# Kernel optimization log

Hardware: AMD Instinct MI355X
Metric: run time of the kernel (lower is better)

## Reference

```python
import jax, jax.numpy as jnp
import numpy as np

B, N = 16, 128
DN0, DE0, DH = 64, 16, 128  # input node dim, input edge dim, hidden dim


def _gnn2(A, x, e, w_msg, b_msg, w_node, b_node):
    """One GNN2 layer on dense batched graphs.
    A: [B,N,N] adjacency mask, x: [B,N,Dn], e: [B,N,N,De].
    Message/new-edge: relu(Linear([x_i, x_j, e_ij])) masked by A.
    New node: relu(Linear([x, sum_j msg_ij])).
    The concat-Linear is decomposed into three matmuls to avoid
    materializing the [B,N,N,2Dn+De] concat tensor.
    """
    Dn = x.shape[-1]
    Wi, Wj, We = w_msg[:Dn], w_msg[Dn:2 * Dn], w_msg[2 * Dn:]
    xi = x @ Wi                                   # [B,N,Do]
    xj = x @ Wj                                   # [B,N,Do]
    msg = jax.nn.relu(xi[:, :, None, :] + xj[:, None, :, :] + e @ We + b_msg)
    msg = msg * A[..., None]                      # mask non-edges -> new edge_attr [B,N,N,Do]
    agg = msg.sum(axis=2)                         # scatter-sum over neighbors j -> [B,N,Do]
    Wx, Wa = w_node[:Dn], w_node[Dn:]
    x_new = jax.nn.relu(x @ Wx + agg @ Wa + b_node)
    return x_new, msg


def setup_inputs() -> dict:
    key = jax.random.key(0)
    ks = iter(jax.random.split(key, 32))
    s = 0.05
    inp = {
        "edge_index": jax.random.randint(next(ks), (B, N, N), 0, 2, dtype=jnp.int32),
        "x": jax.random.normal(next(ks), (B, N, DN0), dtype=jnp.float32),
        "edge_attr": jax.random.normal(next(ks), (B, N, N, DE0), dtype=jnp.float32),
    }
    def w(shape):
        return s * jax.random.normal(next(ks), shape, dtype=jnp.float32)
    # layer 0: node_in=64, edge_in=16 -> 128
    inp["w_msg_0"], inp["b_msg_0"] = w((2 * DN0 + DE0, DH)), w((DH,))
    inp["w_node_0"], inp["b_node_0"] = w((DN0 + DH, DH)), w((DH,))
    # layers 1,2: 128 -> 128
    for l in (1, 2):
        inp[f"w_msg_{l}"], inp[f"b_msg_{l}"] = w((2 * DH + DH, DH)), w((DH,))
        inp[f"w_node_{l}"], inp[f"b_node_{l}"] = w((DH + DH, DH)), w((DH,))
    # head mlp: 128 -> 128 -> 128 -> 1
    inp["w_h1"], inp["b_h1"] = w((DH, DH)), w((DH,))
    inp["w_h2"], inp["b_h2"] = w((DH, DH)), w((DH,))
    inp["w_h3"], inp["b_h3"] = w((DH, 1)), w((1,))
    return inp


def reference(edge_index, x, edge_attr,
              w_msg_0, b_msg_0, w_node_0, b_node_0,
              w_msg_1, b_msg_1, w_node_1, b_node_1,
              w_msg_2, b_msg_2, w_node_2, b_node_2,
              w_h1, b_h1, w_h2, b_h2, w_h3, b_h3):
    A = edge_index.astype(jnp.float32)
    x = x.astype(jnp.float32)
    # layer 0
    x, e = _gnn2(A, x, edge_attr, w_msg_0, b_msg_0, w_node_0, b_node_0)
    # middle layer with 0.5 residual blend
    x_, e_ = _gnn2(A, x, e, w_msg_1, b_msg_1, w_node_1, b_node_1)
    x = 0.5 * (x + x_)
    e = 0.5 * (e + e_)
    # last layer
    x, e = _gnn2(A, x, e, w_msg_2, b_msg_2, w_node_2, b_node_2)
    # edge_mean readout + MLP head
    h = e.mean(axis=(1, 2))                       # [B, DH]
    h = jax.nn.relu(h @ w_h1 + b_h1)
    h = jax.nn.relu(h @ w_h2 + b_h2)
    out = h @ w_h3 + b_h3                         # [B, 1]
    return out.squeeze(-1)                        # [B]
```

## Files before the change

### kernel.cpp

```cpp
#include <hip/hip_runtime.h>

constexpr int B = 16, N = 128, D = 128, DN0 = 64, DE0 = 16;

typedef _Float16 half8 __attribute__((ext_vector_type(8)));
typedef _Float16 half4 __attribute__((ext_vector_type(4)));
typedef float floatx4 __attribute__((ext_vector_type(4)));
typedef float floatx16 __attribute__((ext_vector_type(16)));

__device__ __forceinline__ void gld16(const _Float16* g, _Float16* l) {
  __builtin_amdgcn_global_load_lds(
      (const __attribute__((address_space(1))) void*)g,
      (__attribute__((address_space(3))) void*)l, 16, 0, 0);
}

__global__ __launch_bounds__(128) void k_wprep(
    const float* __restrict__ wm1, const float* __restrict__ wm2,
    _Float16* __restrict__ weT1, _Float16* __restrict__ weT2) {
  const int bid = blockIdx.x;
  const int layer = bid >> 7, c = bid & 127;
  const int k = threadIdx.x;
  const float* src = layer ? wm2 : wm1;
  _Float16* dst = layer ? weT2 : weT1;
  dst[c * D + k] = (_Float16)src[(2 * D + k) * D + c];
}

__global__ __launch_bounds__(256) void k_pre0(
    const float* __restrict__ x, const float* __restrict__ wm0,
    const float* __restrict__ bm0,
    float* __restrict__ xi0, float* __restrict__ xj0) {
  const int row = blockIdx.x;
  const int t = threadIdx.x;
  const int half = t >> 7, c = t & 127;
  __shared__ float xr[DN0];
  if (t < DN0) xr[t] = x[(size_t)row * DN0 + t];
  __syncthreads();
  float a = half ? 0.f : bm0[c];
  const float* wb = wm0 + half * DN0 * D;
  #pragma unroll 8
  for (int k = 0; k < DN0; ++k) a = fmaf(xr[k], wb[k * D + c], a);
  (half ? xj0 : xi0)[(size_t)row * D + c] = a;
}

__global__ __launch_bounds__(256) void k_edge0(
    const int* __restrict__ ei, const float* __restrict__ eattr,
    const float* __restrict__ wm0, const float* __restrict__ x0,
    const float* __restrict__ xi0, const float* __restrict__ xj0,
    const float* __restrict__ wn0, const float* __restrict__ bn0,
    const float* __restrict__ wm1, const float* __restrict__ bm1,
    _Float16* __restrict__ msg0, float* __restrict__ x1,
    float* __restrict__ xi1, float* __restrict__ xj1) {
  const int row = blockIdx.x;
  const int b = row >> 7;
  const int t = threadIdx.x;
  const int c8 = (t & 15) * 8, jr = t >> 4;

  __shared__ float eb[N * 20];
  __shared__ float w_t[DE0][D];
  __shared__ float amask[N];
  __shared__ float xi_r[D];
  __shared__ float sX0[DN0], sAgg[D], sPart[2][D], sX1[D];
  float* hp = eb;

  const float4* esrc = (const float4*)(eattr + (size_t)row * N * DE0);
  const float4* wsrc = (const float4*)(wm0 + 2 * DN0 * D);
  #pragma unroll
  for (int u = 0; u < 2; ++u) {
    const int idx4 = u * 256 + t;
    const int j = idx4 >> 2;
    const int k4 = (idx4 & 3) * 4;
    *(float4*)&eb[j * 20 + k4] = esrc[idx4];
    ((float4*)&w_t[0][0])[idx4] = wsrc[idx4];
  }
  if (t < N) {
    amask[t] = (float)ei[(size_t)row * N + t];
    xi_r[t] = xi0[(size_t)row * D + t];
  } else if (t < N + DN0) {
    sX0[t - N] = x0[(size_t)row * DN0 + (t - N)];
  }
  __syncthreads();

  float acc[8][8] = {};
  #pragma unroll 4
  for (int k = 0; k < DE0; ++k) {
    float av[8];
    #pragma unroll
    for (int p = 0; p < 8; ++p) av[p] = eb[(16 * p + jr) * 20 + k];
    const floatx4 wv0 = *(const floatx4*)&w_t[k][c8];
    const floatx4 wv1 = *(const floatx4*)&w_t[k][c8 + 4];
    #pragma unroll
    for (int p = 0; p < 8; ++p)
      #pragma unroll
      for (int q = 0; q < 4; ++q) {
        acc[p][q]     = fmaf(av[p], wv0[q], acc[p][q]);
        acc[p][4 + q] = fmaf(av[p], wv1[q], acc[p][4 + q]);
      }
  }

  float acc8[8] = {};
  const float* xjb = xj0 + (size_t)b * N * D;
  _Float16* mrow = msg0 + (size_t)row * N * D;
  const floatx4 xiv0 = *(const floatx4*)&xi_r[c8];
  const floatx4 xiv1 = *(const floatx4*)&xi_r[c8 + 4];
  #pragma unroll
  for (int p = 0; p < 8; ++p) {
    const int j = 16 * p + jr;
    const float am = amask[j];
    const floatx4 xjv0 = *(const floatx4*)&xjb[j * D + c8];
    const floatx4 xjv1 = *(const floatx4*)&xjb[j * D + c8 + 4];
    half8 hv;
    #pragma unroll
    for (int q = 0; q < 4; ++q) {
      float v0 = fmaxf(xiv0[q] + xjv0[q] + acc[p][q], 0.f) * am;
      float v1 = fmaxf(xiv1[q] + xjv1[q] + acc[p][4 + q], 0.f) * am;
      hv[q] = (_Float16)v0;
      hv[4 + q] = (_Float16)v1;
      acc8[q] += v0;
      acc8[4 + q] += v1;
    }
    if (am != 0.f)
      *(half8*)&mrow[j * D + (((t & 15) ^ jr) << 3)] = hv;
  }

  __syncthreads();
  #pragma unroll
  for (int q = 0; q < 8; ++q) hp[(jr * 16 + (t & 15)) * 8 + q] = acc8[q];
  __syncthreads();
  if (t < D) {
    float s = 0.f;
    #pragma unroll
    for (int g = 0; g < 16; ++g) s += hp[(g * 16 + (t >> 3)) * 8 + (t & 7)];
    sAgg[t] = s;
  }
  __syncthreads();

  const int half = t >> 7, c = t & 127;
  {
    float a;
    if (half == 0) {
      a = bn0[c];
      #pragma unroll 8
      for (int k = 0; k < DN0; ++k) a = fmaf(sX0[k], wn0[k * D + c], a);
      #pragma unroll 8
      for (int k = 0; k < 32; ++k) a = fmaf(sAgg[k], wn0[(DN0 + k) * D + c], a);
    } else {
      a = 0.f;
      #pragma unroll 8
      for (int k = 32; k < D; ++k) a = fmaf(sAgg[k], wn0[(DN0 + k) * D + c], a);
    }
    sPart[half][c] = a;
  }
  __syncthreads();
  if (t < D) {
    const float v = fmaxf(sPart[0][t] + sPart[1][t], 0.f);
    x1[(size_t)row * D + t] = v;
    sX1[t] = v;
  }
  __syncthreads();

  {
    float aa = half ? 0.f : bm1[c];
    const float* wh = wm1 + half * D * D;
    #pragma unroll 8
    for (int k = 0; k < D; ++k) aa = fmaf(sX1[k], wh[k * D + c], aa);
    (half ? xj1 : xi1)[(size_t)row * D + c] = aa;
  }
}

__global__ __launch_bounds__(256) void k_node1(
    const float* __restrict__ x1, const float* __restrict__ agg1,
    const float* __restrict__ wn1, const float* __restrict__ bn1,
    const float* __restrict__ wm2, const float* __restrict__ bm2,
    float* __restrict__ xi2, float* __restrict__ xj2) {
  const int row = blockIdx.x;
  const int t = threadIdx.x;
  const int half = t >> 7, c = t & 127;
  __shared__ float x1r[D], ar[D], sPart[2][D], x2r[D];
  if (t < D) x1r[t] = x1[(size_t)row * D + t];
  else ar[t - D] = agg1[(size_t)row * D + (t - D)];
  __syncthreads();
  {
    float a;
    if (half == 0) {
      a = bn1[c];
      #pragma unroll 8
      for (int k = 0; k < D; ++k) a = fmaf(x1r[k], wn1[k * D + c], a);
    } else {
      a = 0.f;
      #pragma unroll 8
      for (int k = 0; k < D; ++k) a = fmaf(ar[k], wn1[(D + k) * D + c], a);
    }
    sPart[half][c] = a;
  }
  __syncthreads();
  if (t < D)
    x2r[t] = 0.5f * (x1r[t] + fmaxf(sPart[0][t] + sPart[1][t], 0.f));
  __syncthreads();
  {
    float aa = half ? 0.f : bm2[c];
    const float* wh = wm2 + half * D * D;
    #pragma unroll 8
    for (int k = 0; k < D; ++k) aa = fmaf(x2r[k], wh[k * D + c], aa);
    (half ? xj2 : xi2)[(size_t)row * D + c] = aa;
  }
}

__global__ __launch_bounds__(256, 3) void k_mid(
    const int* __restrict__ ei, const _Float16* __restrict__ weT1,
    const _Float16* __restrict__ weT2,
    const float* __restrict__ xi, const float* __restrict__ xj,
    _Float16* __restrict__ em,
    float* __restrict__ agg1) {
  const int row = blockIdx.x;
  const int b = row >> 7;
  const int t = threadIdx.x;
  const int w = t >> 6;
  const int lane = t & 63;
  const int l31 = lane & 31;
  const int l15 = lane & 15;
  const int hl = lane >> 5;

  __shared__ _Float16 sE[N * D];
  __shared__ float sMask[N];

  const _Float16* gsrc = em + (size_t)row * N * D;
  #pragma unroll
  for (int u = 0; u < 8; ++u) {
    const int seg = (u * 4 + w) * 512;
    gld16(gsrc + seg + lane * 8, &sE[seg]);
  }

  half8 a1[8];
  #pragma unroll
  for (int ks = 0; ks < 8; ++ks)
    a1[ks] = *(const half8*)(weT1 + (32 * w + l31) * D + 16 * ks + 8 * hl);

  floatx4 xiv[4];
  #pragma unroll
  for (int g = 0; g < 4; ++g)
    xiv[g] = *(const floatx4*)&xi[(size_t)row * D + 32 * w + 8 * g + 4 * hl];
  if (t < N) sMask[t] = (float)ei[(size_t)row * N + t];

  __syncthreads();

  float am[4];
  #pragma unroll
  for (int jt = 0; jt < 4; ++jt) am[jt] = sMask[32 * jt + l31];

  const floatx16 vzero = {0.f,0.f,0.f,0.f,0.f,0.f,0.f,0.f,
                          0.f,0.f,0.f,0.f,0.f,0.f,0.f,0.f};
  floatx16 acc[4];
  #pragma unroll
  for (int jt = 0; jt < 4; ++jt) acc[jt] = vzero;
  #pragma unroll
  for (int ks = 0; ks < 8; ++ks)
    #pragma unroll
    for (int jt = 0; jt < 4; ++jt) {
      const half8 bv = *(const half8*)
          &sE[(32 * jt + l31) * D + (((2 * ks + hl) ^ l15) << 3)];
      acc[jt] = __builtin_amdgcn_mfma_f32_32x32x16_f16(a1[ks], bv, acc[jt], 0, 0, 0);
    }

  __syncthreads();

  const float* xjb = xj + (size_t)b * N * D;
  floatx4 hacc[4];
  #pragma unroll
  for (int g = 0; g < 4; ++g) hacc[g] = (floatx4){0.f, 0.f, 0.f, 0.f};
  #pragma unroll
  for (int jt = 0; jt < 4; ++jt) {
    const int j = 32 * jt + l31;
    #pragma unroll
    for (int g = 0; g < 4; ++g) {
      const int cofs = 32 * w + 8 * g + 4 * hl;
      const int hidx = j * D + (((4 * w + g) ^ l15) << 3) + 4 * hl;
      const floatx4 xjv = *(const floatx4*)&xjb[j * D + cofs];
      const half4 m0 = *(const half4*)&sE[hidx];
      half4 mid;
      floatx4 m1;
      #pragma unroll
      for (int r = 0; r < 4; ++r) {
        const float v = xiv[g][r] + xjv[r] + acc[jt][4 * g + r];
        m1[r] = fmaxf(v, 0.f) * am[jt];
        mid[r] = (_Float16)(0.5f * ((float)m0[r] + m1[r]));
      }
      *(half4*)&sE[hidx] = mid;
      hacc[g] += m1;
    }
  }

  #pragma unroll
  for (int m = 1; m < 32; m <<= 1)
    #pragma unroll
    for (int g = 0; g < 4; ++g)
      #pragma unroll
      for (int r = 0; r < 4; ++r)
        hacc[g][r] += __shfl_xor(hacc[g][r], m, 64);
  if (l31 == 0) {
    #pragma unroll
    for (int g = 0; g < 4; ++g)
      *(floatx4*)&agg1[(size_t)row * D + 32 * w + 8 * g + 4 * hl] = hacc[g];
  }

  half8 a2[8];
  #pragma unroll
  for (int ks = 0; ks < 8; ++ks)
    a2[ks] = *(const half8*)(weT2 + (32 * w + l31) * D + 16 * ks + 8 * hl);

  __syncthreads();

  #pragma unroll
  for (int jt = 0; jt < 4; ++jt) acc[jt] = vzero;
  #pragma unroll
  for (int ks = 0; ks < 8; ++ks)
    #pragma unroll
    for (int jt = 0; jt < 4; ++jt) {
      const half8 bv = *(const half8*)
          &sE[(32 * jt + l31) * D + (((2 * ks + hl) ^ l15) << 3)];
      acc[jt] = __builtin_amdgcn_mfma_f32_32x32x16_f16(a2[ks], bv, acc[jt], 0, 0, 0);
    }

  __syncthreads();

  #pragma unroll
  for (int jt = 0; jt < 4; ++jt) {
    const int j = 32 * jt + l31;
    #pragma unroll
    for (int g = 0; g < 4; ++g) {
      const int hidx = j * D + (((4 * w + g) ^ l15) << 3) + 4 * hl;
      half4 tv;
      #pragma unroll
      for (int r = 0; r < 4; ++r) tv[r] = (_Float16)acc[jt][4 * g + r];
      *(half4*)&sE[hidx] = tv;
    }
  }

  __syncthreads();

  uint4* gdst = (uint4*)(em + (size_t)row * N * D);
  const uint4* ls = (const uint4*)sE;
  #pragma unroll
  for (int u = 0; u < 8; ++u) {
    const int idx4 = u * 256 + t;
    const int j = u * 16 + (t >> 4);
    if (sMask[j] != 0.f) gdst[idx4] = ls[idx4];
  }
}

__global__ __launch_bounds__(256) void k_fin(
    const int* __restrict__ ei, const _Float16* __restrict__ t2,
    const float* __restrict__ xi, const float* __restrict__ xj,
    float* __restrict__ rowsum) {
  const int row = blockIdx.x;
  const int b = row >> 7;
  const int t = threadIdx.x;
  const int c8 = (t & 15) * 8, jr = t >> 4;

  __shared__ float sMask[N];
  __shared__ float hp[16][16][8];
  if (t < N) sMask[t] = (float)ei[(size_t)row * N + t];
  float xiv[8];
  *(floatx4*)&xiv[0] = *(const floatx4*)&xi[row * D + c8];
  *(floatx4*)&xiv[4] = *(const floatx4*)&xi[row * D + c8 + 4];
  __syncthreads();

  const _Float16* src = t2 + (size_t)row * N * D;
  const float* xjb = xj + (size_t)b * N * D;
  float acc8[8] = {};
  #pragma unroll
  for (int u = 0; u < 8; ++u) {
    const int j = u * 16 + jr;
    if (sMask[j] != 0.f) {
      const half8 tv = *(const half8*)(src + j * D + (((t & 15) ^ jr) << 3));
      const floatx4 xj0 = *(const floatx4*)&xjb[j * D + c8];
      const floatx4 xj1 = *(const floatx4*)&xjb[j * D + c8 + 4];
      #pragma unroll
      for (int r = 0; r < 4; ++r) {
        acc8[r]     += fmaxf(xiv[r] + xj0[r] + (float)tv[r], 0.f);
        acc8[4 + r] += fmaxf(xiv[4 + r] + xj1[r] + (float)tv[4 + r], 0.f);
      }
    }
  }
  #pragma unroll
  for (int k = 0; k < 8; ++k) hp[jr][t & 15][k] = acc8[k];
  __syncthreads();
  if (t < D) {
    float s = 0.f;
    #pragma unroll
    for (int g = 0; g < 16; ++g) s += hp[g][t >> 3][t & 7];
    rowsum[row * D + t] = s;
  }
}

__global__ __launch_bounds__(128) void k_head(
    const float* __restrict__ rowsum,
    const float* __restrict__ w1, const float* __restrict__ b1,
    const float* __restrict__ w2, const float* __restrict__ b2,
    const float* __restrict__ w3, const float* __restrict__ b3,
    float* __restrict__ out) {
  const int b = blockIdx.x;
  const int c = threadIdx.x;
  __shared__ float hr[D], h1r[D], h2r[D];
  const float* rs = rowsum + (size_t)b * N * D;
  float s = 0.f;
  for (int i = 0; i < N; ++i) s += rs[i * D + c];
  hr[c] = s * (1.f / (N * N));
  __syncthreads();
  float a = b1[c];
  #pragma unroll 8
  for (int k = 0; k < D; ++k) a = fmaf(hr[k], w1[k * D + c], a);
  h1r[c] = fmaxf(a, 0.f);
  __syncthreads();
  a = b2[c];
  #pragma unroll 8
  for (int k = 0; k < D; ++k) a = fmaf(h1r[k], w2[k * D + c], a);
  h2r[c] = fmaxf(a, 0.f);
  __syncthreads();
  hr[c] = h2r[c] * w3[c];
  __syncthreads();
  if (c == 0) {
    float s2 = b3[0];
    for (int k = 0; k < D; ++k) s2 += hr[k];
    out[b] = s2;
  }
}

extern "C" void kernel_launch(void* const* d_in, const int* in_sizes, int n_in,
                              void* d_out, int out_size, void* d_ws, size_t ws_size,
                              hipStream_t stream) {
  const int*   ei  = (const int*)d_in[0];
  const float* x0  = (const float*)d_in[1];
  const float* ea  = (const float*)d_in[2];
  const float* wm0 = (const float*)d_in[3];
  const float* bm0 = (const float*)d_in[4];
  const float* wn0 = (const float*)d_in[5];
  const float* bn0 = (const float*)d_in[6];
  const float* wm1 = (const float*)d_in[7];
  const float* bm1 = (const float*)d_in[8];
  const float* wn1 = (const float*)d_in[9];
  const float* bn1 = (const float*)d_in[10];
  const float* wm2 = (const float*)d_in[11];
  const float* bm2 = (const float*)d_in[12];
  const float* wh1 = (const float*)d_in[15];
  const float* bh1 = (const float*)d_in[16];
  const float* wh2 = (const float*)d_in[17];
  const float* bh2 = (const float*)d_in[18];
  const float* wh3 = (const float*)d_in[19];
  const float* bh3 = (const float*)d_in[20];
  float* out = (float*)d_out;

  _Float16* msg0h = (_Float16*)d_ws;
  _Float16* weT1  = msg0h + (size_t)B * N * N * D;
  _Float16* weT2  = weT1 + D * D;
  float* f = (float*)(weT2 + D * D);
  size_t off = 0;
  const size_t R = (size_t)B * N * D;
  float* xi0  = f + off; off += R;
  float* xj0  = f + off; off += R;
  float* x1   = f + off; off += R;
  float* xi1  = f + off; off += R;
  float* xj1  = f + off; off += R;
  float* agg1 = f + off; off += R;
  float* xi2  = f + off; off += R;
  float* xj2  = f + off; off += R;
  float* rsum = f + off; off += R;

  const int rows = B * N;
  k_wprep<<<256, 128, 0, stream>>>(wm1, wm2, weT1, weT2);
  k_pre0 <<<rows, 256, 0, stream>>>(x0, wm0, bm0, xi0, xj0);
  k_edge0<<<rows, 256, 0, stream>>>(ei, ea, wm0, x0, xi0, xj0,
                                    wn0, bn0, wm1, bm1,
                                    msg0h, x1, xi1, xj1);
  k_mid  <<<rows, 256, 0, stream>>>(ei, weT1, weT2, xi1, xj1, msg0h, agg1);
  k_node1<<<rows, 256, 0, stream>>>(x1, agg1, wn1, bn1, wm2, bm2, xi2, xj2);
  k_fin  <<<rows, 256, 0, stream>>>(ei, msg0h, xi2, xj2, rsum);
  k_head <<<B,    128, 0, stream>>>(rsum, wh1, bh1, wh2, bh2, wh3, bh3, out);
}
```

Baseline: 229.1 us.

## Use MFMA for layer-0 edge projection and stage msg0 through LDS

Replaces the scalar FP32 FMA edge-attribute projection in k_edge0 with a single 32x32x16 f16 MFMA per 32-row tile, using a new FP16 transposed copy of the edge weight prepared in k_wprep. Messages are written swizzled into a shared-memory tile, and the neighbour aggregation becomes a wave shuffle reduction. The tile is then copied to global memory with coalesced 16-byte stores, skipping masked rows. k_mid's launch-bounds occupancy hint also drops from 3 to 2 blocks per SM. Edge attributes and weights are rounded to FP16, which costs some precision, and the 32KB LDS tile may reduce occupancy of k_edge0.

```diff
diff --git a/kernel.cpp b/kernel.cpp
--- a/kernel.cpp
+++ b/kernel.cpp
@@ -14,14 +14,20 @@
 }
 
 __global__ __launch_bounds__(128) void k_wprep(
-    const float* __restrict__ wm1, const float* __restrict__ wm2,
+    const float* __restrict__ wm0, const float* __restrict__ wm1,
+    const float* __restrict__ wm2, _Float16* __restrict__ weT0,
     _Float16* __restrict__ weT1, _Float16* __restrict__ weT2) {
   const int bid = blockIdx.x;
-  const int layer = bid >> 7, c = bid & 127;
   const int k = threadIdx.x;
-  const float* src = layer ? wm2 : wm1;
-  _Float16* dst = layer ? weT2 : weT1;
-  dst[c * D + k] = (_Float16)src[(2 * D + k) * D + c];
+  if (bid < 256) {
+    const int layer = bid >> 7, c = bid & 127;
+    const float* src = layer ? wm2 : wm1;
+    _Float16* dst = layer ? weT2 : weT1;
+    dst[c * D + k] = (_Float16)src[(2 * D + k) * D + c];
+  } else {
+    const int k16 = bid - 256;
+    weT0[k * DE0 + k16] = (_Float16)wm0[(2 * DN0 + k16) * D + k];
+  }
 }
 
 __global__ __launch_bounds__(256) void k_pre0(
@@ -43,7 +49,7 @@
 
 __global__ __launch_bounds__(256) void k_edge0(
     const int* __restrict__ ei, const float* __restrict__ eattr,
-    const float* __restrict__ wm0, const float* __restrict__ x0,
+    const _Float16* __restrict__ weT0, const float* __restrict__ x0,
     const float* __restrict__ xi0, const float* __restrict__ xj0,
     const float* __restrict__ wn0, const float* __restrict__ bn0,
     const float* __restrict__ wm1, const float* __restrict__ bm1,
@@ -52,86 +58,94 @@
   const int row = blockIdx.x;
   const int b = row >> 7;
   const int t = threadIdx.x;
-  const int c8 = (t & 15) * 8, jr = t >> 4;
-
-  __shared__ float eb[N * 20];
-  __shared__ float w_t[DE0][D];
-  __shared__ float amask[N];
-  __shared__ float xi_r[D];
+  const int w = t >> 6, lane = t & 63;
+  const int l31 = lane & 31, l15 = lane & 15, hl = lane >> 5;
+
+  __shared__ _Float16 sEa[N * 20];
+  __shared__ _Float16 sE[N * D];
+  __shared__ float sMask[N];
   __shared__ float sX0[DN0], sAgg[D], sPart[2][D], sX1[D];
-  float* hp = eb;
 
   const float4* esrc = (const float4*)(eattr + (size_t)row * N * DE0);
-  const float4* wsrc = (const float4*)(wm0 + 2 * DN0 * D);
   #pragma unroll
   for (int u = 0; u < 2; ++u) {
     const int idx4 = u * 256 + t;
-    const int j = idx4 >> 2;
-    const int k4 = (idx4 & 3) * 4;
-    *(float4*)&eb[j * 20 + k4] = esrc[idx4];
-    ((float4*)&w_t[0][0])[idx4] = wsrc[idx4];
-  }
-  if (t < N) {
-    amask[t] = (float)ei[(size_t)row * N + t];
-    xi_r[t] = xi0[(size_t)row * D + t];
-  } else if (t < N + DN0) {
-    sX0[t - N] = x0[(size_t)row * DN0 + (t - N)];
-  }
-  __syncthreads();
-
-  float acc[8][8] = {};
-  #pragma unroll 4
-  for (int k = 0; k < DE0; ++k) {
-    float av[8];
-    #pragma unroll
-    for (int p = 0; p < 8; ++p) av[p] = eb[(16 * p + jr) * 20 + k];
-    const floatx4 wv0 = *(const floatx4*)&w_t[k][c8];
-    const floatx4 wv1 = *(const floatx4*)&w_t[k][c8 + 4];
-    #pragma unroll
-    for (int p = 0; p < 8; ++p)
-      #pragma unroll
-      for (int q = 0; q < 4; ++q) {
-        acc[p][q]     = fmaf(av[p], wv0[q], acc[p][q]);
-        acc[p][4 + q] = fmaf(av[p], wv1[q], acc[p][4 + q]);
+    const int j = idx4 >> 2, k4 = (idx4 & 3) * 4;
+    const float4 v = esrc[idx4];
+    half4 hv;
+    hv[0] = (_Float16)v.x; hv[1] = (_Float16)v.y;
+    hv[2] = (_Float16)v.z; hv[3] = (_Float16)v.w;
+    *(half4*)&sEa[j * 20 + k4] = hv;
+  }
+  if (t < N) sMask[t] = (float)ei[(size_t)row * N + t];
+  else if (t < N + DN0) sX0[t - N] = x0[(size_t)row * DN0 + (t - N)];
+
+  const half8 a0 = *(const half8*)(weT0 + (32 * w + l31) * DE0 + 8 * hl);
+  floatx4 xiv[4];
+  #pragma unroll
+  for (int g = 0; g < 4; ++g)
+    xiv[g] = *(const floatx4*)&xi0[(size_t)row * D + 32 * w + 8 * g + 4 * hl];
+  __syncthreads();
+
+  float am[4];
+  #pragma unroll
+  for (int jt = 0; jt < 4; ++jt) am[jt] = sMask[32 * jt + l31];
+
+  const floatx16 vzero = {0.f,0.f,0.f,0.f,0.f,0.f,0.f,0.f,
+                          0.f,0.f,0.f,0.f,0.f,0.f,0.f,0.f};
+  floatx16 acc[4];
+  #pragma unroll
+  for (int jt = 0; jt < 4; ++jt) {
+    const half8 bv = *(const half8*)&sEa[(32 * jt + l31) * 20 + 8 * hl];
+    acc[jt] = __builtin_amdgcn_mfma_f32_32x32x16_f16(a0, bv, vzero, 0, 0, 0);
+  }
+
+  const float* xjb = xj0 + (size_t)b * N * D;
+  floatx4 hacc[4];
+  #pragma unroll
+  for (int g = 0; g < 4; ++g) hacc[g] = (floatx4){0.f, 0.f, 0.f, 0.f};
+  #pragma unroll
+  for (int jt = 0; jt < 4; ++jt) {
+    const int j = 32 * jt + l31;
+    #pragma unroll
+    for (int g = 0; g < 4; ++g) {
+      const int cofs = 32 * w + 8 * g + 4 * hl;
+      const int hidx = j * D + (((4 * w + g) ^ l15) << 3) + 4 * hl;
+      const floatx4 xjv = *(const floatx4*)&xjb[j * D + cofs];
+      half4 hv;
+      floatx4 m1;
+      #pragma unroll
+      for (int r = 0; r < 4; ++r) {
+        m1[r] = fmaxf(xiv[g][r] + xjv[r] + acc[jt][4 * g + r], 0.f) * am[jt];
+        hv[r] = (_Float16)m1[r];
       }
-  }
-
-  float acc8[8] = {};
-  const float* xjb = xj0 + (size_t)b * N * D;
-  _Float16* mrow = msg0 + (size_t)row * N * D;
-  const floatx4 xiv0 = *(const floatx4*)&xi_r[c8];
-  const floatx4 xiv1 = *(const floatx4*)&xi_r[c8 + 4];
-  #pragma unroll
-  for (int p = 0; p < 8; ++p) {
-    const int j = 16 * p + jr;
-    const float am = amask[j];
-    const floatx4 xjv0 = *(const floatx4*)&xjb[j * D + c8];
-    const floatx4 xjv1 = *(const floatx4*)&xjb[j * D + c8 + 4];
-    half8 hv;
-    #pragma unroll
-    for (int q = 0; q < 4; ++q) {
-      float v0 = fmaxf(xiv0[q] + xjv0[q] + acc[p][q], 0.f) * am;
-      float v1 = fmaxf(xiv1[q] + xjv1[q] + acc[p][4 + q], 0.f) * am;
-      hv[q] = (_Float16)v0;
-      hv[4 + q] = (_Float16)v1;
-      acc8[q] += v0;
-      acc8[4 + q] += v1;
-    }
-    if (am != 0.f)
-      *(half8*)&mrow[j * D + (((t & 15) ^ jr) << 3)] = hv;
-  }
-
-  __syncthreads();
-  #pragma unroll
-  for (int q = 0; q < 8; ++q) hp[(jr * 16 + (t & 15)) * 8 + q] = acc8[q];
-  __syncthreads();
-  if (t < D) {
-    float s = 0.f;
-    #pragma unroll
-    for (int g = 0; g < 16; ++g) s += hp[(g * 16 + (t >> 3)) * 8 + (t & 7)];
-    sAgg[t] = s;
-  }
-  __syncthreads();
+      *(half4*)&sE[hidx] = hv;
+      hacc[g] += m1;
+    }
+  }
+
+  #pragma unroll
+  for (int m = 1; m < 32; m <<= 1)
+    #pragma unroll
+    for (int g = 0; g < 4; ++g)
+      #pragma unroll
+      for (int r = 0; r < 4; ++r)
+        hacc[g][r] += __shfl_xor(hacc[g][r], m, 64);
+  if (l31 == 0) {
+    #pragma unroll
+    for (int g = 0; g < 4; ++g)
+      *(floatx4*)&sAgg[32 * w + 8 * g + 4 * hl] = hacc[g];
+  }
+  __syncthreads();
+
+  uint4* gdst = (uint4*)(msg0 + (size_t)row * N * D);
+  const uint4* ls = (const uint4*)sE;
+  #pragma unroll
+  for (int u = 0; u < 8; ++u) {
+    const int idx4 = u * 256 + t;
+    const int j = u * 16 + (t >> 4);
+    if (sMask[j] != 0.f) gdst[idx4] = ls[idx4];
+  }
 
   const int half = t >> 7, c = t & 127;
   {
@@ -204,7 +218,7 @@
   }
 }
 
-__global__ __launch_bounds__(256, 3) void k_mid(
+__global__ __launch_bounds__(256, 2) void k_mid(
     const int* __restrict__ ei, const _Float16* __restrict__ weT1,
     const _Float16* __restrict__ weT2,
     const float* __restrict__ xi, const float* __restrict__ xj,
@@ -451,7 +465,8 @@
   _Float16* msg0h = (_Float16*)d_ws;
   _Float16* weT1  = msg0h + (size_t)B * N * N * D;
   _Float16* weT2  = weT1 + D * D;
-  float* f = (float*)(weT2 + D * D);
+  _Float16* weT0  = weT2 + D * D;
+  float* f = (float*)(weT0 + D * DE0);
   size_t off = 0;
   const size_t R = (size_t)B * N * D;
   float* xi0  = f + off; off += R;
@@ -465,9 +480,9 @@
   float* rsum = f + off; off += R;
 
   const int rows = B * N;
-  k_wprep<<<256, 128, 0, stream>>>(wm1, wm2, weT1, weT2);
+  k_wprep<<<272, 128, 0, stream>>>(wm0, wm1, wm2, weT0, weT1, weT2);
   k_pre0 <<<rows, 256, 0, stream>>>(x0, wm0, bm0, xi0, xj0);
-  k_edge0<<<rows, 256, 0, stream>>>(ei, ea, wm0, x0, xi0, xj0,
+  k_edge0<<<rows, 256, 0, stream>>>(ei, ea, weT0, x0, xi0, xj0,
                                     wn0, bn0, wm1, bm1,
                                     msg0h, x1, xi1, xj1);
   k_mid  <<<rows, 256, 0, stream>>>(ei, weT1, weT2, xi1, xj1, msg0h, agg1);
```

After: 234.9 us. +2.5%, slower.

## Fuse weight prep into pre0 kernel and node-1 update into mid kernel

Applied to the files above, without the earlier changes.

Merges the fp16 weight-transpose kernel into the layer-0 projection kernel by appending extra blocks, and folds the layer-1 node update plus layer-2 xi/xj projection into the tail of k_mid. Aggregates stay in shared memory instead of going through global memory. This saves two launches and a global round trip. In exchange, k_mid's launch bound drops from 3 to 2 blocks per SM and it now runs a serial per-row matvec tail that reads weights from global memory, which may reduce the overlap of its MFMA phase.

```diff
diff --git a/kernel.cpp b/kernel.cpp
--- a/kernel.cpp
+++ b/kernel.cpp
@@ -13,32 +13,34 @@
       (__attribute__((address_space(3))) void*)l, 16, 0, 0);
 }
 
-__global__ __launch_bounds__(128) void k_wprep(
-    const float* __restrict__ wm1, const float* __restrict__ wm2,
+__global__ __launch_bounds__(256) void k_pre(
+    const float* __restrict__ x, const float* __restrict__ wm0,
+    const float* __restrict__ bm0, const float* __restrict__ wm1,
+    const float* __restrict__ wm2,
+    float* __restrict__ xi0, float* __restrict__ xj0,
     _Float16* __restrict__ weT1, _Float16* __restrict__ weT2) {
   const int bid = blockIdx.x;
-  const int layer = bid >> 7, c = bid & 127;
-  const int k = threadIdx.x;
-  const float* src = layer ? wm2 : wm1;
-  _Float16* dst = layer ? weT2 : weT1;
-  dst[c * D + k] = (_Float16)src[(2 * D + k) * D + c];
-}
-
-__global__ __launch_bounds__(256) void k_pre0(
-    const float* __restrict__ x, const float* __restrict__ wm0,
-    const float* __restrict__ bm0,
-    float* __restrict__ xi0, float* __restrict__ xj0) {
-  const int row = blockIdx.x;
   const int t = threadIdx.x;
-  const int half = t >> 7, c = t & 127;
-  __shared__ float xr[DN0];
-  if (t < DN0) xr[t] = x[(size_t)row * DN0 + t];
-  __syncthreads();
-  float a = half ? 0.f : bm0[c];
-  const float* wb = wm0 + half * DN0 * D;
-  #pragma unroll 8
-  for (int k = 0; k < DN0; ++k) a = fmaf(xr[k], wb[k * D + c], a);
-  (half ? xj0 : xi0)[(size_t)row * D + c] = a;
+  if (bid < B * N) {
+    const int row = bid;
+    const int half = t >> 7, c = t & 127;
+    __shared__ float xr[DN0];
+    if (t < DN0) xr[t] = x[(size_t)row * DN0 + t];
+    __syncthreads();
+    float a = half ? 0.f : bm0[c];
+    const float* wb = wm0 + half * DN0 * D;
+    #pragma unroll 8
+    for (int k = 0; k < DN0; ++k) a = fmaf(xr[k], wb[k * D + c], a);
+    (half ? xj0 : xi0)[(size_t)row * D + c] = a;
+  } else {
+    const int g = (bid - B * N) * 256 + t;
+    const int layer = g >> 14;
+    const int rem = g & 16383;
+    const int c = rem >> 7, k = rem & 127;
+    const float* src = layer ? wm2 : wm1;
+    _Float16* dst = layer ? weT2 : weT1;
+    dst[rem] = (_Float16)src[(2 * D + k) * D + c];
+  }
 }
 
 __global__ __launch_bounds__(256) void k_edge0(
@@ -166,50 +168,15 @@
   }
 }
 
-__global__ __launch_bounds__(256) void k_node1(
-    const float* __restrict__ x1, const float* __restrict__ agg1,
-    const float* __restrict__ wn1, const float* __restrict__ bn1,
-    const float* __restrict__ wm2, const float* __restrict__ bm2,
-    float* __restrict__ xi2, float* __restrict__ xj2) {
-  const int row = blockIdx.x;
-  const int t = threadIdx.x;
-  const int half = t >> 7, c = t & 127;
-  __shared__ float x1r[D], ar[D], sPart[2][D], x2r[D];
-  if (t < D) x1r[t] = x1[(size_t)row * D + t];
-  else ar[t - D] = agg1[(size_t)row * D + (t - D)];
-  __syncthreads();
-  {
-    float a;
-    if (half == 0) {
-      a = bn1[c];
-      #pragma unroll 8
-      for (int k = 0; k < D; ++k) a = fmaf(x1r[k], wn1[k * D + c], a);
-    } else {
-      a = 0.f;
-      #pragma unroll 8
-      for (int k = 0; k < D; ++k) a = fmaf(ar[k], wn1[(D + k) * D + c], a);
-    }
-    sPart[half][c] = a;
-  }
-  __syncthreads();
-  if (t < D)
-    x2r[t] = 0.5f * (x1r[t] + fmaxf(sPart[0][t] + sPart[1][t], 0.f));
-  __syncthreads();
-  {
-    float aa = half ? 0.f : bm2[c];
-    const float* wh = wm2 + half * D * D;
-    #pragma unroll 8
-    for (int k = 0; k < D; ++k) aa = fmaf(x2r[k], wh[k * D + c], aa);
-    (half ? xj2 : xi2)[(size_t)row * D + c] = aa;
-  }
-}
-
-__global__ __launch_bounds__(256, 3) void k_mid(
+__global__ __launch_bounds__(256, 2) void k_mid(
     const int* __restrict__ ei, const _Float16* __restrict__ weT1,
     const _Float16* __restrict__ weT2,
     const float* __restrict__ xi, const float* __restrict__ xj,
+    const float* __restrict__ x1,
+    const float* __restrict__ wn1, const float* __restrict__ bn1,
+    const float* __restrict__ wm2, const float* __restrict__ bm2,
     _Float16* __restrict__ em,
-    float* __restrict__ agg1) {
+    float* __restrict__ xi2, float* __restrict__ xj2) {
   const int row = blockIdx.x;
   const int b = row >> 7;
   const int t = threadIdx.x;
@@ -221,6 +188,7 @@
 
   __shared__ _Float16 sE[N * D];
   __shared__ float sMask[N];
+  __shared__ float sAgg[D], sX1[D], sPart[2][D], sX2[D];
 
   const _Float16* gsrc = em + (size_t)row * N * D;
   #pragma unroll
@@ -239,6 +207,7 @@
   for (int g = 0; g < 4; ++g)
     xiv[g] = *(const floatx4*)&xi[(size_t)row * D + 32 * w + 8 * g + 4 * hl];
   if (t < N) sMask[t] = (float)ei[(size_t)row * N + t];
+  else if (t < N + D) sX1[t - N] = x1[(size_t)row * D + (t - N)];
 
   __syncthreads();
 
@@ -298,7 +267,7 @@
   if (l31 == 0) {
     #pragma unroll
     for (int g = 0; g < 4; ++g)
-      *(floatx4*)&agg1[(size_t)row * D + 32 * w + 8 * g + 4 * hl] = hacc[g];
+      *(floatx4*)&sAgg[32 * w + 8 * g + 4 * hl] = hacc[g];
   }
 
   half8 a2[8];
@@ -343,6 +312,32 @@
     const int idx4 = u * 256 + t;
     const int j = u * 16 + (t >> 4);
     if (sMask[j] != 0.f) gdst[idx4] = ls[idx4];
+  }
+
+  const int half = t >> 7, c = t & 127;
+  {
+    float a;
+    if (half == 0) {
+      a = bn1[c];
+      #pragma unroll 8
+      for (int k = 0; k < D; ++k) a = fmaf(sX1[k], wn1[k * D + c], a);
+    } else {
+      a = 0.f;
+      #pragma unroll 8
+      for (int k = 0; k < D; ++k) a = fmaf(sAgg[k], wn1[(D + k) * D + c], a);
+    }
+    sPart[half][c] = a;
+  }
+  __syncthreads();
+  if (t < D)
+    sX2[t] = 0.5f * (sX1[t] + fmaxf(sPart[0][t] + sPart[1][t], 0.f));
+  __syncthreads();
+  {
+    float aa = half ? 0.f : bm2[c];
+    const float* wh = wm2 + half * D * D;
+    #pragma unroll 8
+    for (int k = 0; k < D; ++k) aa = fmaf(sX2[k], wh[k * D + c], aa);
+    (half ? xj2 : xi2)[(size_t)row * D + c] = aa;
   }
 }
 
@@ -459,19 +454,19 @@
   float* x1   = f + off; off += R;
   float* xi1  = f + off; off += R;
   float* xj1  = f + off; off += R;
-  float* agg1 = f + off; off += R;
   float* xi2  = f + off; off += R;
   float* xj2  = f + off; off += R;
   float* rsum = f + off; off += R;
 
   const int rows = B * N;
-  k_wprep<<<256, 128, 0, stream>>>(wm1, wm2, weT1, weT2);
-  k_pre0 <<<rows, 256, 0, stream>>>(x0, wm0, bm0, xi0, xj0);
+  k_pre  <<<rows + 128, 256, 0, stream>>>(x0, wm0, bm0, wm1, wm2,
+                                          xi0, xj0, weT1, weT2);
   k_edge0<<<rows, 256, 0, stream>>>(ei, ea, wm0, x0, xi0, xj0,
                                     wn0, bn0, wm1, bm1,
                                     msg0h, x1, xi1, xj1);
-  k_mid  <<<rows, 256, 0, stream>>>(ei, weT1, weT2, xi1, xj1, msg0h, agg1);
-  k_node1<<<rows, 256, 0, stream>>>(x1, agg1, wn1, bn1, wm2, bm2, xi2, xj2);
+  k_mid  <<<rows, 256, 0, stream>>>(ei, weT1, weT2, xi1, xj1, x1,
+                                    wn1, bn1, wm2, bm2,
+                                    msg0h, xi2, xj2);
   k_fin  <<<rows, 256, 0, stream>>>(ei, msg0h, xi2, xj2, rsum);
   k_head <<<B,    128, 0, stream>>>(rsum, wh1, bh1, wh2, bh2, wh3, bh3, out);
 }
```

After: 228.0 us. No clear change (-0.5%).
